# Kernel optimization log

Measured on AMD Instinct MI355X. Metric: run time of the kernel, lower is better.

Reference implementation:

```python
import jax, jax.numpy as jnp
import numpy as np

B = 2048
HID = 256      # hidden_dim (latent)
COND = 128     # cond_dim
NCH = 64       # n_chars
MAXLEN = 128   # max_len
R = 256        # recurrent_dim


def setup_inputs() -> dict:
    key = jax.random.key(0)
    ks = jax.random.split(key, 10)
    s = 0.05
    return {
        "z": jax.random.normal(ks[0], (B, HID), jnp.float32),
        "x_cond": jax.random.normal(ks[1], (B, COND), jnp.float32),
        # latent_to_hidden: Linear(hidden_dim + cond_dim -> recurrent_dim)
        "W_lh": jax.random.normal(ks[2], (R, HID + COND), jnp.float32) * s,
        "b_lh": jax.random.normal(ks[3], (R,), jnp.float32) * s,
        # GRU (single layer): weights in PyTorch gate order [r, z, n]
        "W_ih": jax.random.normal(ks[4], (3 * R, R), jnp.float32) * s,
        "W_hh": jax.random.normal(ks[5], (3 * R, R), jnp.float32) * s,
        "b_ih": jax.random.normal(ks[6], (3 * R,), jnp.float32) * s,
        "b_hh": jax.random.normal(ks[7], (3 * R,), jnp.float32) * s,
        # output_layer: Linear(recurrent_dim -> n_chars)
        "W_out": jax.random.normal(ks[8], (NCH, R), jnp.float32) * s,
        "b_out": jax.random.normal(ks[9], (NCH,), jnp.float32) * s,
    }


def _gru_cell(x, h, W_ih, W_hh, b_ih, b_hh):
    # PyTorch GRU cell: gates ordered [reset, update, new]
    gi = x @ W_ih.T + b_ih          # (B, 3R)
    gh = h @ W_hh.T + b_hh          # (B, 3R)
    i_r, i_z, i_n = jnp.split(gi, 3, axis=-1)
    h_r, h_z, h_n = jnp.split(gh, 3, axis=-1)
    r = jax.nn.sigmoid(i_r + h_r)
    u = jax.nn.sigmoid(i_z + h_z)
    n = jnp.tanh(i_n + r * h_n)
    return (1.0 - u) * n + u * h


def reference(z, x_cond, W_lh, b_lh, W_ih, W_hh, b_ih, b_hh, W_out, b_out):
    # Generation branch (teacher_force_inputs is None), dropout=0.0
    zc = jnp.concatenate([z, x_cond], axis=1)          # (B, HID+COND)
    h0 = zc @ W_lh.T + b_lh                            # (B, R), gru_depth=1
    x0 = jnp.zeros((z.shape[0], R), dtype=z.dtype)     # initial input step

    def step(carry, _):
        h, xin = carry
        hn = _gru_cell(xin, h, W_ih, W_hh, b_ih, b_hh)  # (B, R)
        logits = hn @ W_out.T + b_out                   # (B, NCH)
        return (hn, hn), logits                         # next input = GRU output

    (_, _), ys = jax.lax.scan(step, (h0, x0), None, length=MAXLEN)
    return jnp.transpose(ys, (1, 0, 2))                 # (B, MAXLEN, NCH)
```

## Files before the change

kernel.cpp:

```cpp
#include <hip/hip_runtime.h>
#include <hip/hip_bf16.h>

#define BATCH 2048
#define NCH 64
#define MAXLEN 128
#define RDIM 256

#define WCAT_OFF 0
#define WHH0_OFF 262144
#define WLH_OFF  524288
#define WOUT_OFF 622592
#define BCAT_OFF 638976
#define BCAT0_OFF 640000

__global__ void prep_kernel(const float* __restrict__ W_lh,
                            const float* __restrict__ W_ih, const float* __restrict__ W_hh,
                            const float* __restrict__ b_ih, const float* __restrict__ b_hh,
                            const float* __restrict__ W_out, float* __restrict__ ws) {
    int gid = blockIdx.x * blockDim.x + threadIdx.x;
    if (gid < 384 * 256) {
        int k = gid >> 8, u = gid & 255;
        ws[WLH_OFF + gid] = W_lh[u * 384 + k];
    }
    if (gid < 65536) {
        int k = gid >> 8, u = gid & 255;
        float ir = W_ih[u * 256 + k], iz = W_ih[(256 + u) * 256 + k], inw = W_ih[(512 + u) * 256 + k];
        float hr = W_hh[u * 256 + k], hz = W_hh[(256 + u) * 256 + k], hnw = W_hh[(512 + u) * 256 + k];
        int base = WCAT_OFF + k * 1024 + u * 4;
        ws[base + 0] = ir + hr; ws[base + 1] = iz + hz; ws[base + 2] = inw; ws[base + 3] = hnw;
        base = WHH0_OFF + k * 1024 + u * 4;
        ws[base + 0] = hr; ws[base + 1] = hz; ws[base + 2] = hnw; ws[base + 3] = 0.0f;
    }
    if (gid < 16384) {
        int o = gid & 63, k = gid >> 6;
        ws[WOUT_OFF + k * 64 + o] = W_out[o * 256 + k];
    }
    if (gid < 256) {
        int u = gid;
        float bir = b_ih[u], biz = b_ih[256 + u];
        float bhr = b_hh[u], bhz = b_hh[256 + u], bhn = b_hh[512 + u];
        int base = BCAT_OFF + u * 4;
        ws[base + 0] = bir + bhr; ws[base + 1] = biz + bhz; ws[base + 2] = b_ih[512 + u]; ws[base + 3] = bhn;
        base = BCAT0_OFF + u * 4;
        ws[base + 0] = bir + bhr; ws[base + 1] = biz + bhz; ws[base + 2] = bhn; ws[base + 3] = 0.0f;
    }
}

__device__ __forceinline__ float sigm(float x)   { return 1.0f / (1.0f + __expf(-x)); }
__device__ __forceinline__ float tanh_f(float x) { return 1.0f - 2.0f / (1.0f + __expf(2.0f * x)); }

__global__ __launch_bounds__(1024, 1)
void gru_persist(const float* __restrict__ z, const float* __restrict__ xc,
                 const float* __restrict__ b_lh, const float* __restrict__ b_ih,
                 const float* __restrict__ b_out_g,
                 const float* __restrict__ ws, float* __restrict__ out) {
    __shared__ __align__(16) float lds_h[8 * 256];
    __shared__ __align__(16) float4 pbufv[4 * 6 * 256];
    __shared__ float lbuf[1024];

    const int tid = threadIdx.x;
    const int u   = tid & 255;
    const int q   = __builtin_amdgcn_readfirstlane(tid >> 8);
    const int b0  = blockIdx.x * 8;

    float* zcs = (float*)pbufv;
    for (int idx = tid; idx < 8 * 384; idx += 1024) {
        int i = idx / 384, k = idx - i * 384;
        zcs[idx] = (k < 256) ? z[(b0 + i) * 256 + k] : xc[(b0 + i) * 128 + (k - 256)];
    }
    __syncthreads();

    float h_own0, h_own1;
    {
        float a0 = b_lh[u], a1 = a0;
        const float* Wlh = ws + WLH_OFF + u;
        const float* zr0 = zcs + (2 * q) * 384;
        const float* zr1 = zr0 + 384;
#pragma unroll 2
        for (int k4 = 0; k4 < 96; ++k4) {
            int k = 4 * k4;
            float w0 = Wlh[(k + 0) * 256];
            float w1 = Wlh[(k + 1) * 256];
            float w2 = Wlh[(k + 2) * 256];
            float w3 = Wlh[(k + 3) * 256];
            const float4 v0 = *(const float4*)(zr0 + k);
            const float4 v1 = *(const float4*)(zr1 + k);
            a0 += v0.x * w0 + v0.y * w1 + v0.z * w2 + v0.w * w3;
            a1 += v1.x * w0 + v1.y * w1 + v1.z * w2 + v1.w * w3;
        }
        h_own0 = a0; h_own1 = a1;
        lds_h[(2 * q) * 256 + u] = a0;
        lds_h[(2 * q + 1) * 256 + u] = a1;
    }
    __syncthreads();

    const float4* Wcat  = (const float4*)(ws + WCAT_OFF);
    const float4* Whh0v = (const float4*)(ws + WHH0_OFF);
    const float4  bc1   = ((const float4*)(ws + BCAT_OFF))[u];
    const float4  bc0v  = ((const float4*)(ws + BCAT0_OFF))[u];
    const float   bin_c = b_ih[512 + u];

    int ro[8];
#pragma unroll
    for (int jj = 0; jj < 8; ++jj) ro[jj] = (((2 * q + jj) & 7) << 8);

    const int lkh = tid & 1;
    const float* hrow_base = lds_h + ((tid >> 1) >> 6) * 256 + lkh * 128;
    const float* wcolT = ws + WOUT_OFF + lkh * 128 * 64 + ((tid >> 1) & 63);
    const int co = tid & 63, cr = tid >> 6;
    const float bout = b_out_g[co];
    float* outp = out + (long)b0 * MAXLEN * NCH;

    for (int st = 0; st < MAXLEN; ++st) {
        const float4* Wp = st ? Wcat : Whh0v;
        float ax[8], ay[8], az[8], aw[8];
#pragma unroll
        for (int jj = 0; jj < 8; ++jj) { ax[jj] = 0.f; ay[jj] = 0.f; az[jj] = 0.f; aw[jj] = 0.f; }

        const float4* wbase = Wp + (q * 64) * 256 + u;
        const float*  hbase = lds_h + q * 64;

#pragma unroll 2
        for (int k4 = 0; k4 < 16; ++k4) {
            const float4 w0 = wbase[(4 * k4 + 0) * 256];
            const float4 w1 = wbase[(4 * k4 + 1) * 256];
            const float4 w2 = wbase[(4 * k4 + 2) * 256];
            const float4 w3 = wbase[(4 * k4 + 3) * 256];
#pragma unroll
            for (int jj = 0; jj < 8; ++jj) {
                const float4 hv = *(const float4*)(hbase + ro[jj] + 4 * k4);
                ax[jj] += hv.x * w0.x; ay[jj] += hv.x * w0.y; az[jj] += hv.x * w0.z; aw[jj] += hv.x * w0.w;
                ax[jj] += hv.y * w1.x; ay[jj] += hv.y * w1.y; az[jj] += hv.y * w1.z; aw[jj] += hv.y * w1.w;
                ax[jj] += hv.z * w2.x; ay[jj] += hv.z * w2.y; az[jj] += hv.z * w2.z; aw[jj] += hv.z * w2.w;
                ax[jj] += hv.w * w3.x; ay[jj] += hv.w * w3.y; az[jj] += hv.w * w3.z; aw[jj] += hv.w * w3.w;
            }
        }

        {
            float4* pb = pbufv + q * 6 * 256 + u;
#pragma unroll
            for (int j = 0; j < 6; ++j)
                pb[j * 256] = make_float4(ax[j + 2], ay[j + 2], az[j + 2], aw[j + 2]);
        }

        if (st) {
            float l = 0.f;
#pragma unroll 8
            for (int kk = 0; kk < 128; ++kk) l += hrow_base[kk] * wcolT[kk * 64];
            lbuf[tid] = l;
        }

        __syncthreads();

#pragma unroll
        for (int qq = 0; qq < 4; ++qq) {
            if (qq != q) {
                const int j0 = (2 * q - 2 * qq - 2) & 7;
                const float4 p0 = pbufv[(qq * 6 + j0) * 256 + u];
                const float4 p1 = pbufv[(qq * 6 + j0 + 1) * 256 + u];
                ax[0] += p0.x; ay[0] += p0.y; az[0] += p0.z; aw[0] += p0.w;
                ax[1] += p1.x; ay[1] += p1.y; az[1] += p1.z; aw[1] += p1.w;
            }
        }
        float hn0, hn1;
        if (st == 0) {
            float r0 = sigm(ax[0] + bc0v.x), z0 = sigm(ay[0] + bc0v.y);
            float n0 = tanh_f(bin_c + r0 * (az[0] + bc0v.z));
            hn0 = (1.f - z0) * n0 + z0 * h_own0;
            float r1 = sigm(ax[1] + bc0v.x), z1 = sigm(ay[1] + bc0v.y);
            float n1 = tanh_f(bin_c + r1 * (az[1] + bc0v.z));
            hn1 = (1.f - z1) * n1 + z1 * h_own1;
        } else {
            float r0 = sigm(ax[0] + bc1.x), z0 = sigm(ay[0] + bc1.y);
            float n0 = tanh_f(az[0] + bc1.z + r0 * (aw[0] + bc1.w));
            hn0 = (1.f - z0) * n0 + z0 * h_own0;
            float r1 = sigm(ax[1] + bc1.x), z1 = sigm(ay[1] + bc1.y);
            float n1 = tanh_f(az[1] + bc1.z + r1 * (aw[1] + bc1.w));
            hn1 = (1.f - z1) * n1 + z1 * h_own1;
        }
        lds_h[(2 * q) * 256 + u] = hn0;
        lds_h[(2 * q + 1) * 256 + u] = hn1;
        h_own0 = hn0; h_own1 = hn1;

        if (st && tid < 512) {
            float l = lbuf[2 * tid] + lbuf[2 * tid + 1] + bout;
            outp[(long)cr * MAXLEN * NCH + (st - 1) * NCH + co] = l;
        }
        __syncthreads();
    }

    {
        float l = 0.f;
#pragma unroll 8
        for (int kk = 0; kk < 128; ++kk) l += hrow_base[kk] * wcolT[kk * 64];
        lbuf[tid] = l;
    }
    __syncthreads();
    if (tid < 512) {
        float l = lbuf[2 * tid] + lbuf[2 * tid + 1] + bout;
        outp[(long)cr * MAXLEN * NCH + (MAXLEN - 1) * NCH + co] = l;
    }
}

extern "C" void kernel_launch(void* const* d_in, const int* in_sizes, int n_in,
                              void* d_out, int out_size, void* d_ws, size_t ws_size,
                              hipStream_t stream) {
    const float* z     = (const float*)d_in[0];
    const float* xcond = (const float*)d_in[1];
    const float* W_lh  = (const float*)d_in[2];
    const float* b_lh  = (const float*)d_in[3];
    const float* W_ih  = (const float*)d_in[4];
    const float* W_hh  = (const float*)d_in[5];
    const float* b_ih  = (const float*)d_in[6];
    const float* b_hh  = (const float*)d_in[7];
    const float* W_out = (const float*)d_in[8];
    const float* b_out = (const float*)d_in[9];
    float* out = (float*)d_out;
    float* ws  = (float*)d_ws;

    hipLaunchKernelGGL(prep_kernel, dim3(384), dim3(256), 0, stream,
                       W_lh, W_ih, W_hh, b_ih, b_hh, W_out, ws);
    hipLaunchKernelGGL(gru_persist, dim3(256), dim3(1024), 0, stream,
                       z, xcond, b_lh, b_ih, b_out, ws, out);
}
```

Baseline: 3.333 ms.

## Retile GRU recurrent matmul to two units per thread with four rows

Reorganizes the per-step recurrent GEMM so each thread computes two hidden units for four batch rows instead of one unit for eight rows. The weight layout is interleaved by unit pairs, and weight loads are software-pipelined by prefetching the next A-half while the B-half is computed. The change is meant to cut LDS reads of h per FMA and raise global weight-load reuse. The cross-k-group reduction through shared memory is rearranged to match, and the output-projection dot product now uses float4 h reads with four partial sums. Register pressure and reduction traffic rise in exchange.

```diff
diff --git a/kernel.cpp b/kernel.cpp
--- a/kernel.cpp
+++ b/kernel.cpp
@@ -26,9 +26,10 @@
         int k = gid >> 8, u = gid & 255;
         float ir = W_ih[u * 256 + k], iz = W_ih[(256 + u) * 256 + k], inw = W_ih[(512 + u) * 256 + k];
         float hr = W_hh[u * 256 + k], hz = W_hh[(256 + u) * 256 + k], hnw = W_hh[(512 + u) * 256 + k];
-        int base = WCAT_OFF + k * 1024 + u * 4;
+        int up = u >> 1, half = u & 1;
+        int base = WCAT_OFF + (k * 128 + up) * 8 + half * 4;
         ws[base + 0] = ir + hr; ws[base + 1] = iz + hz; ws[base + 2] = inw; ws[base + 3] = hnw;
-        base = WHH0_OFF + k * 1024 + u * 4;
+        base = WHH0_OFF + (k * 128 + up) * 8 + half * 4;
         ws[base + 0] = hr; ws[base + 1] = hz; ws[base + 2] = hnw; ws[base + 3] = 0.0f;
     }
     if (gid < 16384) {
@@ -49,19 +50,27 @@
 __device__ __forceinline__ float sigm(float x)   { return 1.0f / (1.0f + __expf(-x)); }
 __device__ __forceinline__ float tanh_f(float x) { return 1.0f - 2.0f / (1.0f + __expf(2.0f * x)); }
 
+__device__ __forceinline__ void fma4(float4& a, float s, const float4 b) {
+    a.x += s * b.x; a.y += s * b.y; a.z += s * b.z; a.w += s * b.w;
+}
+
 __global__ __launch_bounds__(1024, 1)
 void gru_persist(const float* __restrict__ z, const float* __restrict__ xc,
                  const float* __restrict__ b_lh, const float* __restrict__ b_ih,
                  const float* __restrict__ b_out_g,
                  const float* __restrict__ ws, float* __restrict__ out) {
     __shared__ __align__(16) float lds_h[8 * 256];
-    __shared__ __align__(16) float4 pbufv[4 * 6 * 256];
+    __shared__ __align__(16) float4 pbufv[2 * 12 * 256];
     __shared__ float lbuf[1024];
 
     const int tid = threadIdx.x;
-    const int u   = tid & 255;
-    const int q   = __builtin_amdgcn_readfirstlane(tid >> 8);
+    const int up  = tid & 127;
+    const int rg  = __builtin_amdgcn_readfirstlane((tid >> 7) & 1);
+    const int kg  = __builtin_amdgcn_readfirstlane(tid >> 8);
     const int b0  = blockIdx.x * 8;
+    const int u0  = 2 * up;
+    const int r_own = rg * 4 + kg;
+    const int col = rg * 128 + up;
 
     float* zcs = (float*)pbufv;
     for (int idx = tid; idx < 8 * 384; idx += 1024) {
@@ -72,37 +81,30 @@
 
     float h_own0, h_own1;
     {
-        float a0 = b_lh[u], a1 = a0;
-        const float* Wlh = ws + WLH_OFF + u;
-        const float* zr0 = zcs + (2 * q) * 384;
-        const float* zr1 = zr0 + 384;
-#pragma unroll 2
-        for (int k4 = 0; k4 < 96; ++k4) {
-            int k = 4 * k4;
-            float w0 = Wlh[(k + 0) * 256];
-            float w1 = Wlh[(k + 1) * 256];
-            float w2 = Wlh[(k + 2) * 256];
-            float w3 = Wlh[(k + 3) * 256];
-            const float4 v0 = *(const float4*)(zr0 + k);
-            const float4 v1 = *(const float4*)(zr1 + k);
-            a0 += v0.x * w0 + v0.y * w1 + v0.z * w2 + v0.w * w3;
-            a1 += v1.x * w0 + v1.y * w1 + v1.z * w2 + v1.w * w3;
+        float a0 = b_lh[u0], a1 = b_lh[u0 + 1];
+        const float* Wlh = ws + WLH_OFF + u0;
+        const float* zr = zcs + r_own * 384;
+#pragma unroll 4
+        for (int k = 0; k < 384; ++k) {
+            const float2 wv = *(const float2*)&Wlh[k * 256];
+            float hvv = zr[k];
+            a0 += hvv * wv.x; a1 += hvv * wv.y;
         }
         h_own0 = a0; h_own1 = a1;
-        lds_h[(2 * q) * 256 + u] = a0;
-        lds_h[(2 * q + 1) * 256 + u] = a1;
+        *(float2*)&lds_h[r_own * 256 + u0] = make_float2(a0, a1);
     }
     __syncthreads();
 
-    const float4* Wcat  = (const float4*)(ws + WCAT_OFF);
-    const float4* Whh0v = (const float4*)(ws + WHH0_OFF);
-    const float4  bc1   = ((const float4*)(ws + BCAT_OFF))[u];
-    const float4  bc0v  = ((const float4*)(ws + BCAT0_OFF))[u];
-    const float   bin_c = b_ih[512 + u];
-
-    int ro[8];
-#pragma unroll
-    for (int jj = 0; jj < 8; ++jj) ro[jj] = (((2 * q + jj) & 7) << 8);
+    const float4  bc1_0 = ((const float4*)(ws + BCAT_OFF))[u0];
+    const float4  bc1_1 = ((const float4*)(ws + BCAT_OFF))[u0 + 1];
+    const float4  bc0_0 = ((const float4*)(ws + BCAT0_OFF))[u0];
+    const float4  bc0_1 = ((const float4*)(ws + BCAT0_OFF))[u0 + 1];
+    const float   binc0 = b_ih[512 + u0], binc1 = b_ih[512 + u0 + 1];
+
+    int ro4[4];
+#pragma unroll
+    for (int jj = 0; jj < 4; ++jj) ro4[jj] = (rg * 4 + ((kg + jj) & 3)) << 8;
+    const int kbase = kg * 64;
 
     const int lkh = tid & 1;
     const float* hrow_base = lds_h + ((tid >> 1) >> 6) * 256 + lkh * 128;
@@ -112,74 +114,95 @@
     float* outp = out + (long)b0 * MAXLEN * NCH;
 
     for (int st = 0; st < MAXLEN; ++st) {
-        const float4* Wp = st ? Wcat : Whh0v;
-        float ax[8], ay[8], az[8], aw[8];
-#pragma unroll
-        for (int jj = 0; jj < 8; ++jj) { ax[jj] = 0.f; ay[jj] = 0.f; az[jj] = 0.f; aw[jj] = 0.f; }
-
-        const float4* wbase = Wp + (q * 64) * 256 + u;
-        const float*  hbase = lds_h + q * 64;
-
+        const float4* Wp4 = (const float4*)(ws + (st ? WCAT_OFF : WHH0_OFF));
+        float4 acc0[4], acc1[4];
+#pragma unroll
+        for (int jj = 0; jj < 4; ++jj) {
+            acc0[jj] = make_float4(0.f, 0.f, 0.f, 0.f);
+            acc1[jj] = make_float4(0.f, 0.f, 0.f, 0.f);
+        }
+
+        float4 A0 = Wp4[((kbase + 0) * 128 + up) * 2];
+        float4 A1 = Wp4[((kbase + 1) * 128 + up) * 2];
+        float4 A2 = Wp4[((kbase + 2) * 128 + up) * 2];
+        float4 A3 = Wp4[((kbase + 3) * 128 + up) * 2];
 #pragma unroll 2
         for (int k4 = 0; k4 < 16; ++k4) {
-            const float4 w0 = wbase[(4 * k4 + 0) * 256];
-            const float4 w1 = wbase[(4 * k4 + 1) * 256];
-            const float4 w2 = wbase[(4 * k4 + 2) * 256];
-            const float4 w3 = wbase[(4 * k4 + 3) * 256];
-#pragma unroll
-            for (int jj = 0; jj < 8; ++jj) {
-                const float4 hv = *(const float4*)(hbase + ro[jj] + 4 * k4);
-                ax[jj] += hv.x * w0.x; ay[jj] += hv.x * w0.y; az[jj] += hv.x * w0.z; aw[jj] += hv.x * w0.w;
-                ax[jj] += hv.y * w1.x; ay[jj] += hv.y * w1.y; az[jj] += hv.y * w1.z; aw[jj] += hv.y * w1.w;
-                ax[jj] += hv.z * w2.x; ay[jj] += hv.z * w2.y; az[jj] += hv.z * w2.z; aw[jj] += hv.z * w2.w;
-                ax[jj] += hv.w * w3.x; ay[jj] += hv.w * w3.y; az[jj] += hv.w * w3.z; aw[jj] += hv.w * w3.w;
-            }
+            const int k = kbase + k4 * 4;
+            float4 B0 = Wp4[((k + 0) * 128 + up) * 2 + 1];
+            float4 B1 = Wp4[((k + 1) * 128 + up) * 2 + 1];
+            float4 B2 = Wp4[((k + 2) * 128 + up) * 2 + 1];
+            float4 B3 = Wp4[((k + 3) * 128 + up) * 2 + 1];
+            float4 hv0 = *(const float4*)&lds_h[ro4[0] + k];
+            float4 hv1 = *(const float4*)&lds_h[ro4[1] + k];
+            float4 hv2 = *(const float4*)&lds_h[ro4[2] + k];
+            float4 hv3 = *(const float4*)&lds_h[ro4[3] + k];
+            fma4(acc0[0], hv0.x, A0); fma4(acc0[0], hv0.y, A1); fma4(acc0[0], hv0.z, A2); fma4(acc0[0], hv0.w, A3);
+            fma4(acc0[1], hv1.x, A0); fma4(acc0[1], hv1.y, A1); fma4(acc0[1], hv1.z, A2); fma4(acc0[1], hv1.w, A3);
+            fma4(acc0[2], hv2.x, A0); fma4(acc0[2], hv2.y, A1); fma4(acc0[2], hv2.z, A2); fma4(acc0[2], hv2.w, A3);
+            fma4(acc0[3], hv3.x, A0); fma4(acc0[3], hv3.y, A1); fma4(acc0[3], hv3.z, A2); fma4(acc0[3], hv3.w, A3);
+            if (k4 < 15) {
+                const int kn = k + 4;
+                A0 = Wp4[((kn + 0) * 128 + up) * 2];
+                A1 = Wp4[((kn + 1) * 128 + up) * 2];
+                A2 = Wp4[((kn + 2) * 128 + up) * 2];
+                A3 = Wp4[((kn + 3) * 128 + up) * 2];
+            }
+            fma4(acc1[0], hv0.x, B0); fma4(acc1[0], hv0.y, B1); fma4(acc1[0], hv0.z, B2); fma4(acc1[0], hv0.w, B3);
+            fma4(acc1[1], hv1.x, B0); fma4(acc1[1], hv1.y, B1); fma4(acc1[1], hv1.z, B2); fma4(acc1[1], hv1.w, B3);
+            fma4(acc1[2], hv2.x, B0); fma4(acc1[2], hv2.y, B1); fma4(acc1[2], hv2.z, B2); fma4(acc1[2], hv2.w, B3);
+            fma4(acc1[3], hv3.x, B0); fma4(acc1[3], hv3.y, B1); fma4(acc1[3], hv3.z, B2); fma4(acc1[3], hv3.w, B3);
         }
 
         {
-            float4* pb = pbufv + q * 6 * 256 + u;
-#pragma unroll
-            for (int j = 0; j < 6; ++j)
-                pb[j * 256] = make_float4(ax[j + 2], ay[j + 2], az[j + 2], aw[j + 2]);
+#pragma unroll
+            for (int jj = 1; jj < 4; ++jj) {
+                const int X = kg * 3 + (jj - 1);
+                pbufv[X * 256 + col] = acc0[jj];
+                pbufv[3072 + X * 256 + col] = acc1[jj];
+            }
         }
 
         if (st) {
-            float l = 0.f;
+            float l0 = 0.f, l1 = 0.f, l2 = 0.f, l3 = 0.f;
 #pragma unroll 8
-            for (int kk = 0; kk < 128; ++kk) l += hrow_base[kk] * wcolT[kk * 64];
-            lbuf[tid] = l;
+            for (int kk = 0; kk < 32; ++kk) {
+                const float4 hval = *(const float4*)&hrow_base[4 * kk];
+                l0 += hval.x * wcolT[(4 * kk + 0) * 64];
+                l1 += hval.y * wcolT[(4 * kk + 1) * 64];
+                l2 += hval.z * wcolT[(4 * kk + 2) * 64];
+                l3 += hval.w * wcolT[(4 * kk + 3) * 64];
+            }
+            lbuf[tid] = (l0 + l1) + (l2 + l3);
         }
 
         __syncthreads();
 
-#pragma unroll
-        for (int qq = 0; qq < 4; ++qq) {
-            if (qq != q) {
-                const int j0 = (2 * q - 2 * qq - 2) & 7;
-                const float4 p0 = pbufv[(qq * 6 + j0) * 256 + u];
-                const float4 p1 = pbufv[(qq * 6 + j0 + 1) * 256 + u];
-                ax[0] += p0.x; ay[0] += p0.y; az[0] += p0.z; aw[0] += p0.w;
-                ax[1] += p1.x; ay[1] += p1.y; az[1] += p1.z; aw[1] += p1.w;
+        float4 s0 = acc0[0], s1 = acc1[0];
+#pragma unroll
+        for (int kq = 0; kq < 4; ++kq) {
+            if (kq != kg) {
+                const int slot = ((kg - kq) & 3) - 1;
+                const int X = kq * 3 + slot;
+                const float4 p0 = pbufv[X * 256 + col];
+                const float4 p1 = pbufv[3072 + X * 256 + col];
+                s0.x += p0.x; s0.y += p0.y; s0.z += p0.z; s0.w += p0.w;
+                s1.x += p1.x; s1.y += p1.y; s1.z += p1.z; s1.w += p1.w;
             }
         }
         float hn0, hn1;
         if (st == 0) {
-            float r0 = sigm(ax[0] + bc0v.x), z0 = sigm(ay[0] + bc0v.y);
-            float n0 = tanh_f(bin_c + r0 * (az[0] + bc0v.z));
-            hn0 = (1.f - z0) * n0 + z0 * h_own0;
-            float r1 = sigm(ax[1] + bc0v.x), z1 = sigm(ay[1] + bc0v.y);
-            float n1 = tanh_f(bin_c + r1 * (az[1] + bc0v.z));
-            hn1 = (1.f - z1) * n1 + z1 * h_own1;
+            float r0 = sigm(s0.x + bc0_0.x), z0 = sigm(s0.y + bc0_0.y);
+            hn0 = (1.f - z0) * tanh_f(binc0 + r0 * (s0.z + bc0_0.z)) + z0 * h_own0;
+            float r1 = sigm(s1.x + bc0_1.x), z1 = sigm(s1.y + bc0_1.y);
+            hn1 = (1.f - z1) * tanh_f(binc1 + r1 * (s1.z + bc0_1.z)) + z1 * h_own1;
         } else {
-            float r0 = sigm(ax[0] + bc1.x), z0 = sigm(ay[0] + bc1.y);
-            float n0 = tanh_f(az[0] + bc1.z + r0 * (aw[0] + bc1.w));
-            hn0 = (1.f - z0) * n0 + z0 * h_own0;
-            float r1 = sigm(ax[1] + bc1.x), z1 = sigm(ay[1] + bc1.y);
-            float n1 = tanh_f(az[1] + bc1.z + r1 * (aw[1] + bc1.w));
-            hn1 = (1.f - z1) * n1 + z1 * h_own1;
-        }
-        lds_h[(2 * q) * 256 + u] = hn0;
-        lds_h[(2 * q + 1) * 256 + u] = hn1;
+            float r0 = sigm(s0.x + bc1_0.x), z0 = sigm(s0.y + bc1_0.y);
+            hn0 = (1.f - z0) * tanh_f(s0.z + bc1_0.z + r0 * (s0.w + bc1_0.w)) + z0 * h_own0;
+            float r1 = sigm(s1.x + bc1_1.x), z1 = sigm(s1.y + bc1_1.y);
+            hn1 = (1.f - z1) * tanh_f(s1.z + bc1_1.z + r1 * (s1.w + bc1_1.w)) + z1 * h_own1;
+        }
+        *(float2*)&lds_h[r_own * 256 + u0] = make_float2(hn0, hn1);
         h_own0 = hn0; h_own1 = hn1;
 
         if (st && tid < 512) {
@@ -190,10 +213,16 @@
     }
 
     {
-        float l = 0.f;
+        float l0 = 0.f, l1 = 0.f, l2 = 0.f, l3 = 0.f;
 #pragma unroll 8
-        for (int kk = 0; kk < 128; ++kk) l += hrow_base[kk] * wcolT[kk * 64];
-        lbuf[tid] = l;
+        for (int kk = 0; kk < 32; ++kk) {
+            const float4 hval = *(const float4*)&hrow_base[4 * kk];
+            l0 += hval.x * wcolT[(4 * kk + 0) * 64];
+            l1 += hval.y * wcolT[(4 * kk + 1) * 64];
+            l2 += hval.z * wcolT[(4 * kk + 2) * 64];
+            l3 += hval.w * wcolT[(4 * kk + 3) * 64];
+        }
+        lbuf[tid] = (l0 + l1) + (l2 + l3);
     }
     __syncthreads();
     if (tid < 512) {
```

Result: slower. 12.28 ms (+268.5%).
